# Kernel tuning notes

Hardware: AMD Instinct MI355X
Metric: run time of the kernel (lower is better)

The kernel has to match this reference:

```python
import jax, jax.numpy as jnp
import numpy as np

B, N, K, C, COND = 8, 2048, 32, 256, 512
LN_EPS = 1e-5


def setup_inputs() -> dict:
    key = jax.random.key(0)
    ks = jax.random.split(key, 8)
    node_feats = jax.random.normal(ks[0], (B, N, C), jnp.float32)
    cond_feats = jax.random.normal(ks[1], (B, COND), jnp.float32)
    W_cond = jax.random.normal(ks[2], (COND, 2 * C), jnp.float32) * 0.02
    b_cond = jnp.zeros((2 * C,), jnp.float32)
    W_film = jax.random.normal(ks[3], (C, C), jnp.float32) * 0.05
    b_film = jnp.zeros((C,), jnp.float32)
    weights = jax.random.uniform(ks[4], (B, N * K, 1), jnp.float32)
    params = jax.random.uniform(ks[5], (B, N * K, 1), jnp.float32)
    coords = jax.random.randint(ks[6], (B * N * K,), 0, B * N, jnp.int64)
    return dict(node_feats=node_feats, cond_feats=cond_feats, W_cond=W_cond,
                b_cond=b_cond, W_film=W_film, b_film=b_film,
                weights=weights, params=params, coords=coords)


def reference(node_feats, cond_feats, W_cond, b_cond, W_film, b_film,
              weights, params, coords):
    # FiLM conditioning: gamma/beta from cond projection  [B, 2C] -> two [B, C]
    gb = cond_feats @ W_cond + b_cond
    gamma, beta = jnp.split(gb, 2, axis=-1)
    gamma = gamma + 1.0
    # film_l: linear -> layernorm (no affine) -> FiLM -> relu
    h = node_feats @ W_film + b_film                      # [B, N, C]
    mu = jnp.mean(h, axis=-1, keepdims=True)
    var = jnp.mean(jnp.square(h - mu), axis=-1, keepdims=True)
    h = (h - mu) * jax.lax.rsqrt(var + LN_EPS)
    new_node_feats = jax.nn.relu(h * gamma[:, None, :] + beta[:, None, :])
    # edge weights: elementwise product, reshape to [B, N, K, 1]
    ew = (weights * params).reshape(B, N, K, 1)
    # gather neighbor feats by flat coords over B*N, then weighted segment-sum over K
    node_j = new_node_feats.reshape(B * N, C)[coords].reshape(B, N, K, C)
    nb_feats = jnp.sum(ew * node_j, axis=2)               # [B, N, C]
    # non-loop op, no GIN: residual add then relu (norm_l is identity)
    return jax.nn.relu(new_node_feats + nb_feats)
```

## Files before the change

kernel.cpp:

```cpp
#include <hip/hip_runtime.h>


typedef unsigned short u16;
typedef unsigned int u32;

typedef __attribute__((ext_vector_type(8))) __bf16 bf16x8;
typedef __attribute__((ext_vector_type(4))) __bf16 bf16x4;
typedef __attribute__((ext_vector_type(4))) float f32x4;
typedef __attribute__((ext_vector_type(2))) float f32x2;
typedef __attribute__((ext_vector_type(4))) u16 u16x4;

__device__ __forceinline__ float b2f(u16 u) {
  union { u32 i; float f; } x; x.i = ((u32)u) << 16; return x.f;
}

__global__ __launch_bounds__(256) void k_prep(const float* __restrict__ Wf,
                                              u16* __restrict__ Wp,
                                              const float* __restrict__ cond,
                                              const float* __restrict__ Wc,
                                              float* __restrict__ gbp) {
  int blk = blockIdx.x;
  int tid = threadIdx.x;
  if (blk < 32) {
    int i0 = blk * 2048 + tid;
    #pragma unroll
    for (int u = 0; u < 8; ++u) {
      int i = i0 + u * 256;
      int j  = i & 7;
      int l  = (i >> 3) & 63;
      int ks = (i >> 9) & 7;
      int ct = i >> 12;
      int k   = ks * 32 + ((l >> 4) << 3) + j;
      int col = ct * 16 + (l & 15);
      __bf16 b = (__bf16)Wf[k * 256 + col];
      Wp[i] = *(u16*)&b;
    }
  } else {
    int idx = blk - 32;
    int kh = idx >> 5;
    int ch = idx & 31;

    __shared__ float cf[2048];
    __shared__ float red[2048];

    #pragma unroll
    for (int u = 0; u < 8; ++u) {
      int i = u * 256 + tid;
      cf[i] = cond[(i >> 8) * 512 + kh * 256 + (i & 255)];
    }
    __syncthreads();

    int col = tid & 15;
    int ks  = tid >> 4;
    float acc[8] = {0.f,0.f,0.f,0.f,0.f,0.f,0.f,0.f};
    #pragma unroll
    for (int t = 0; t < 16; ++t) {
      int kl = ks * 16 + t;
      float wv = Wc[(kh * 256 + kl) * 512 + ch * 16 + col];
      #pragma unroll
      for (int b = 0; b < 8; ++b)
        acc[b] += cf[b * 256 + kl] * wv;
    }
    #pragma unroll
    for (int b = 0; b < 8; ++b)
      red[ks * 128 + b * 16 + col] = acc[b];
    __syncthreads();

    if (tid < 128) {
      float s = 0.f;
      #pragma unroll
      for (int p = 0; p < 16; ++p)
        s += red[p * 128 + tid];
      gbp[(kh * 8 + (tid >> 4)) * 512 + ch * 16 + (tid & 15)] = s;
    }
  }
}

__global__ __launch_bounds__(256) void k_film(const float* __restrict__ A,
                                              const u16* __restrict__ Wp,
                                              const float* __restrict__ bfm,
                                              const float* __restrict__ gbp,
                                              const float* __restrict__ bcond,
                                              u16* __restrict__ nnf) {
  const int tid = threadIdx.x;
  const int l = tid & 63;
  const int w = tid >> 6;
  const int row0 = blockIdx.x * 16;
  const int b = row0 >> 11;

  __shared__ u16 As[16 * 264];
  __shared__ float red[4][4][2][4];

  #pragma unroll
  for (int u = 0; u < 4; ++u) {
    int f = u * 256 + tid;
    int row = f >> 6;
    int col = (f & 63) * 4;
    f32x4 v = *(const f32x4*)(A + (size_t)(row0 + row) * 256 + col);
    bf16x4 pk;
    pk[0] = (__bf16)v.x; pk[1] = (__bf16)v.y;
    pk[2] = (__bf16)v.z; pk[3] = (__bf16)v.w;
    *(bf16x4*)(As + row * 264 + col) = pk;
  }
  __syncthreads();

  f32x4 acc[4];
  #pragma unroll
  for (int c = 0; c < 4; ++c) {
    acc[c].x = 0.f; acc[c].y = 0.f; acc[c].z = 0.f; acc[c].w = 0.f;
  }

  const u16* asrc = As + (l & 15) * 264 + ((l >> 4) << 3);
  const u16* wl = Wp + (size_t)l * 8;

  #pragma unroll
  for (int ks = 0; ks < 8; ++ks) {
    bf16x8 af = *(const bf16x8*)(asrc + ks * 32);
    #pragma unroll
    for (int c = 0; c < 4; ++c) {
      int ct = w * 4 + c;
      bf16x8 bfr = *(const bf16x8*)(wl + ((size_t)(ct * 8 + ks)) * 512);
      acc[c] = __builtin_amdgcn_mfma_f32_16x16x32_bf16(af, bfr, acc[c], 0, 0, 0);
    }
  }

  const int g = l >> 4;
  float s[4] = {0.f, 0.f, 0.f, 0.f};
  float q[4] = {0.f, 0.f, 0.f, 0.f};
  #pragma unroll
  for (int c = 0; c < 4; ++c) {
    float bcol = bfm[(w * 4 + c) * 16 + (l & 15)];
    #pragma unroll
    for (int r = 0; r < 4; ++r) {
      float v = acc[c][r] + bcol;
      acc[c][r] = v;
      s[r] += v;
      q[r] += v * v;
    }
  }
  #pragma unroll
  for (int m = 1; m < 16; m <<= 1) {
    #pragma unroll
    for (int r = 0; r < 4; ++r) {
      s[r] += __shfl_xor(s[r], m);
      q[r] += __shfl_xor(q[r], m);
    }
  }
  if ((l & 15) == 0) {
    #pragma unroll
    for (int r = 0; r < 4; ++r) {
      red[w][g][0][r] = s[r];
      red[w][g][1][r] = q[r];
    }
  }
  __syncthreads();

  float ga[4], be[4];
  #pragma unroll
  for (int c = 0; c < 4; ++c) {
    int col = (w * 4 + c) * 16 + (l & 15);
    ga[c] = gbp[b * 512 + col] + gbp[(8 + b) * 512 + col] + bcond[col] + 1.0f;
    be[c] = gbp[b * 512 + 256 + col] + gbp[(8 + b) * 512 + 256 + col] + bcond[256 + col];
  }

  float mu[4], rs[4];
  #pragma unroll
  for (int r = 0; r < 4; ++r) {
    float ss = red[0][g][0][r] + red[1][g][0][r] + red[2][g][0][r] + red[3][g][0][r];
    float qq = red[0][g][1][r] + red[1][g][1][r] + red[2][g][1][r] + red[3][g][1][r];
    mu[r] = ss * (1.0f / 256.0f);
    float var = qq * (1.0f / 256.0f) - mu[r] * mu[r];
    rs[r] = rsqrtf(var + 1e-5f);
  }

  const int rowb = row0 + (g << 2);
  #pragma unroll
  for (int c = 0; c < 4; ++c) {
    int col = (w * 4 + c) * 16 + (l & 15);
    #pragma unroll
    for (int r = 0; r < 4; ++r) {
      float h = (acc[c][r] - mu[r]) * rs[r];
      float o = fmaxf(h * ga[c] + be[c], 0.f);
      ((__bf16*)nnf)[(size_t)(rowb + r) * 256 + col] = (__bf16)o;
    }
  }
}

__global__ __launch_bounds__(256) void k_gather(const u16* __restrict__ nnf,
                                                const float* __restrict__ wts,
                                                const float* __restrict__ prm,
                                                const int* __restrict__ coords,
                                                float* __restrict__ out) {
  const int q  = blockIdx.x >> 10;
  const int rg = blockIdx.x & 1023;
  const int tid = threadIdx.x;

  __shared__ int   s_idx[512];
  __shared__ float s_ew[512];

  {
    int base = rg * 512 + tid * 2;
    int2  c2 = *(const int2*)(coords + base);
    f32x2 w2 = __builtin_nontemporal_load((const f32x2*)(wts + base));
    f32x2 p2 = __builtin_nontemporal_load((const f32x2*)(prm + base));
    s_idx[tid * 2]     = c2.x;
    s_idx[tid * 2 + 1] = c2.y;
    s_ew[tid * 2]      = w2.x * p2.x;
    s_ew[tid * 2 + 1]  = w2.y * p2.y;
  }
  __syncthreads();

  const int w = tid >> 6;
  const int l = tid & 63;
  const int g = l >> 4;
  const int m = l & 15;
  const int rl = w * 4 + g;
  const int row = rg * 16 + rl;
  const int kbase = rl * 32;
  const u16* colp = nnf + q * 64 + m * 4;

  u16x4 v[32];
  #pragma unroll
  for (int k = 0; k < 32; ++k) {
    int idx = s_idx[kbase + k];
    v[k] = *(const u16x4*)(colp + ((size_t)idx << 8));
  }

  float acc[4] = {0.f, 0.f, 0.f, 0.f};
  #pragma unroll
  for (int k = 0; k < 32; ++k) {
    float wgt = s_ew[kbase + k];
    #pragma unroll
    for (int j = 0; j < 4; ++j)
      acc[j] += wgt * b2f(v[k][j]);
  }

  u16x4 sv = *(const u16x4*)(colp + ((size_t)row << 8));
  f32x4 o;
  o.x = fmaxf(b2f(sv.x) + acc[0], 0.f);
  o.y = fmaxf(b2f(sv.y) + acc[1], 0.f);
  o.z = fmaxf(b2f(sv.z) + acc[2], 0.f);
  o.w = fmaxf(b2f(sv.w) + acc[3], 0.f);
  __builtin_nontemporal_store(o, (f32x4*)(out + (size_t)row * 256 + q * 64 + m * 4));
}

extern "C" void kernel_launch(void* const* d_in, const int* in_sizes, int n_in,
                              void* d_out, int out_size, void* d_ws, size_t ws_size,
                              hipStream_t stream) {
  const float* node = (const float*)d_in[0];
  const float* cond = (const float*)d_in[1];
  const float* Wc   = (const float*)d_in[2];
  const float* bc   = (const float*)d_in[3];
  const float* Wf   = (const float*)d_in[4];
  const float* bf   = (const float*)d_in[5];
  const float* wts  = (const float*)d_in[6];
  const float* prm  = (const float*)d_in[7];
  const int* coords = (const int*)d_in[8];
  float* out = (float*)d_out;

  char* ws = (char*)d_ws;
  float* gbp = (float*)ws;
  u16* Wp    = (u16*)(ws + 32768);
  u16* nnf   = (u16*)(ws + 32768 + 131072);

  k_prep<<<dim3(96), dim3(256), 0, stream>>>(Wf, Wp, cond, Wc, gbp);
  k_film<<<dim3(1024), dim3(256), 0, stream>>>(node, Wp, bf, gbp, bc, nnf);
  k_gather<<<dim3(4096), dim3(256), 0, stream>>>(nnf, wts, prm, coords, out);
}
```

Baseline: 46.31 us.

## Precompute edge weights in prep kernel and load FiLM A operand directly from global

The weights*params product moves into extra blocks of the prep kernel, which write it to a workspace buffer. The gather kernel then reads one array instead of two, which matters because each edge-weight slice is loaded by four column-quarter blocks. The FiLM kernel drops its shared-memory staging and barrier and loads fp32 A fragments straight from global memory, converting to bf16 in registers. The risks are the extra write and read of the 2 MB ew buffer, and less coalesced strided A loads in the FiLM kernel.

Result: slower. 50.22 us (+8.5%).

```diff
diff --git a/kernel.cpp b/kernel.cpp
--- a/kernel.cpp
+++ b/kernel.cpp
@@ -18,7 +18,10 @@
                                               u16* __restrict__ Wp,
                                               const float* __restrict__ cond,
                                               const float* __restrict__ Wc,
-                                              float* __restrict__ gbp) {
+                                              float* __restrict__ gbp,
+                                              const float* __restrict__ wts,
+                                              const float* __restrict__ prm,
+                                              float* __restrict__ ew) {
   int blk = blockIdx.x;
   int tid = threadIdx.x;
   if (blk < 32) {
@@ -35,7 +38,7 @@
       __bf16 b = (__bf16)Wf[k * 256 + col];
       Wp[i] = *(u16*)&b;
     }
-  } else {
+  } else if (blk < 96) {
     int idx = blk - 32;
     int kh = idx >> 5;
     int ch = idx & 31;
@@ -72,6 +75,16 @@
       for (int p = 0; p < 16; ++p)
         s += red[p * 128 + tid];
       gbp[(kh * 8 + (tid >> 4)) * 512 + ch * 16 + (tid & 15)] = s;
+    }
+  } else {
+    int i0 = (blk - 96) * 16384 + tid * 4;
+    #pragma unroll
+    for (int u = 0; u < 16; ++u) {
+      int e = i0 + u * 1024;
+      f32x4 w = *(const f32x4*)(wts + e);
+      f32x4 p = *(const f32x4*)(prm + e);
+      f32x4 r = w * p;
+      *(f32x4*)(ew + e) = r;
     }
   }
 }
@@ -88,34 +101,26 @@
   const int row0 = blockIdx.x * 16;
   const int b = row0 >> 11;
 
-  __shared__ u16 As[16 * 264];
   __shared__ float red[4][4][2][4];
 
-  #pragma unroll
-  for (int u = 0; u < 4; ++u) {
-    int f = u * 256 + tid;
-    int row = f >> 6;
-    int col = (f & 63) * 4;
-    f32x4 v = *(const f32x4*)(A + (size_t)(row0 + row) * 256 + col);
-    bf16x4 pk;
-    pk[0] = (__bf16)v.x; pk[1] = (__bf16)v.y;
-    pk[2] = (__bf16)v.z; pk[3] = (__bf16)v.w;
-    *(bf16x4*)(As + row * 264 + col) = pk;
-  }
-  __syncthreads();
-
   f32x4 acc[4];
   #pragma unroll
   for (int c = 0; c < 4; ++c) {
     acc[c].x = 0.f; acc[c].y = 0.f; acc[c].z = 0.f; acc[c].w = 0.f;
   }
 
-  const u16* asrc = As + (l & 15) * 264 + ((l >> 4) << 3);
+  const float* arow = A + (size_t)(row0 + (l & 15)) * 256 + ((l >> 4) << 3);
   const u16* wl = Wp + (size_t)l * 8;
 
   #pragma unroll
   for (int ks = 0; ks < 8; ++ks) {
-    bf16x8 af = *(const bf16x8*)(asrc + ks * 32);
+    f32x4 a0 = *(const f32x4*)(arow + ks * 32);
+    f32x4 a1 = *(const f32x4*)(arow + ks * 32 + 4);
+    bf16x8 af;
+    af[0] = (__bf16)a0.x; af[1] = (__bf16)a0.y;
+    af[2] = (__bf16)a0.z; af[3] = (__bf16)a0.w;
+    af[4] = (__bf16)a1.x; af[5] = (__bf16)a1.y;
+    af[6] = (__bf16)a1.z; af[7] = (__bf16)a1.w;
     #pragma unroll
     for (int c = 0; c < 4; ++c) {
       int ct = w * 4 + c;
@@ -187,8 +192,7 @@
 }
 
 __global__ __launch_bounds__(256) void k_gather(const u16* __restrict__ nnf,
-                                                const float* __restrict__ wts,
-                                                const float* __restrict__ prm,
+                                                const float* __restrict__ ew,
                                                 const int* __restrict__ coords,
                                                 float* __restrict__ out) {
   const int q  = blockIdx.x >> 10;
@@ -201,12 +205,11 @@
   {
     int base = rg * 512 + tid * 2;
     int2  c2 = *(const int2*)(coords + base);
-    f32x2 w2 = __builtin_nontemporal_load((const f32x2*)(wts + base));
-    f32x2 p2 = __builtin_nontemporal_load((const f32x2*)(prm + base));
+    f32x2 e2 = __builtin_nontemporal_load((const f32x2*)(ew + base));
     s_idx[tid * 2]     = c2.x;
     s_idx[tid * 2 + 1] = c2.y;
-    s_ew[tid * 2]      = w2.x * p2.x;
-    s_ew[tid * 2 + 1]  = w2.y * p2.y;
+    s_ew[tid * 2]      = e2.x;
+    s_ew[tid * 2 + 1]  = e2.y;
   }
   __syncthreads();
 
@@ -261,9 +264,10 @@
   char* ws = (char*)d_ws;
   float* gbp = (float*)ws;
   u16* Wp    = (u16*)(ws + 32768);
-  u16* nnf   = (u16*)(ws + 32768 + 131072);
-
-  k_prep<<<dim3(96), dim3(256), 0, stream>>>(Wf, Wp, cond, Wc, gbp);
+  float* ew  = (float*)(ws + 163840);
+  u16* nnf   = (u16*)(ws + 2260992);
+
+  k_prep<<<dim3(128), dim3(256), 0, stream>>>(Wf, Wp, cond, Wc, gbp, wts, prm, ew);
   k_film<<<dim3(1024), dim3(256), 0, stream>>>(node, Wp, bf, gbp, bc, nnf);
-  k_gather<<<dim3(4096), dim3(256), 0, stream>>>(nnf, wts, prm, coords, out);
-}
+  k_gather<<<dim3(4096), dim3(256), 0, stream>>>(nnf, ew, coords, out);
+}
```
